# Performance work log

Measured on AMD Instinct MI355X. Metric: run time of the kernel, lower is better.

Reference implementation:

```python
import math
import jax, jax.numpy as jnp
import numpy as np

B, N, D, H = 16, 256, 1024, 16
DK = D // H
LAM_ATT, LAM_DIST = 0.33, 0.33
LAM_ADJ = 1.0 - LAM_ATT - LAM_DIST
EPS, NEG_INF = 1e-6, 1e12


def setup_inputs() -> dict:
    key = jax.random.key(0)
    ks = jax.random.split(key, 16)
    inp = {
        'query': jax.random.normal(ks[0], (B, N, D), jnp.float32),
        'key': jax.random.normal(ks[1], (B, N, D), jnp.float32),
        'value': jax.random.normal(ks[2], (B, N, D), jnp.float32),
        'adj_matrix': jax.random.uniform(ks[3], (B, N, N), jnp.float32),
        'distance_matrix': jax.random.uniform(ks[4], (B, N, N), jnp.float32),
        'edges_att': jnp.zeros((1,), jnp.float32),  # unused by forward
    }
    mask = jax.random.randint(ks[5], (B, N), 0, 2, jnp.int32)
    inp['mask'] = mask.at[:, 0].set(1)  # guarantee >=1 valid atom per graph
    scale = 0.02
    inp['Wq'] = jax.random.normal(ks[6], (D, D), jnp.float32) * scale
    inp['bq'] = jnp.zeros((D,), jnp.float32)
    inp['Wk'] = jax.random.normal(ks[7], (D, D), jnp.float32) * scale
    inp['bk'] = jnp.zeros((D,), jnp.float32)
    inp['Wv'] = jax.random.normal(ks[8], (D, D), jnp.float32) * scale
    inp['bv'] = jnp.zeros((D,), jnp.float32)
    inp['Wo'] = jax.random.normal(ks[9], (D, D), jnp.float32) * scale
    inp['bo'] = jnp.zeros((D,), jnp.float32)
    return inp


def reference(query, key, value, adj_matrix, distance_matrix, edges_att, mask,
              Wq, bq, Wk, bk, Wv, bv, Wo, bo):
    b, n, d = query.shape
    proj = lambda x, W, bias: (x @ W + bias).reshape(b, n, H, DK).transpose(0, 2, 1, 3)
    q = proj(query, Wq, bq)   # [B,H,N,DK]
    k = proj(key, Wk, bk)
    v = proj(value, Wv, bv)

    scores = jnp.einsum('bhqd,bhkd->bhqk', q, k) / math.sqrt(DK)
    key_invalid = (mask == 0)[:, None, None, :]          # [B,1,1,N]
    scores = jnp.where(key_invalid, -NEG_INF, scores)
    p_attn = jax.nn.softmax(scores, axis=-1)             # [B,H,N,N]

    # row-normalized adjacency (broadcast over heads instead of repeat)
    p_adj = adj_matrix / (adj_matrix.sum(axis=-1, keepdims=True) + EPS)  # [B,N,N]

    # distance kernel: softmax(-dist) with masked columns sent to +inf
    dist = jnp.where((mask == 0)[:, None, :], jnp.inf, distance_matrix)  # [B,N,N]
    p_dist = jax.nn.softmax(-dist, axis=-1)

    p_weighted = (LAM_ATT * p_attn
                  + LAM_DIST * p_dist[:, None]
                  + LAM_ADJ * p_adj[:, None])            # [B,H,N,N]
    # dropout p=0.0 -> identity

    x = jnp.einsum('bhqk,bhkd->bhqd', p_weighted, v)     # [B,H,N,DK]
    x = x.transpose(0, 2, 1, 3).reshape(b, n, d)
    return x @ Wo + bo
```

## Files before the change

### kernel.cpp

```cpp
#include <hip/hip_runtime.h>
#include <hip/hip_bf16.h>

typedef short short8 __attribute__((ext_vector_type(8)));
typedef short short4v __attribute__((ext_vector_type(4)));
typedef float floatx4 __attribute__((ext_vector_type(4)));

constexpr int BB  = 16;
constexpr int NN  = 256;
constexpr int DD  = 1024;
constexpr int HHc = 16;
constexpr int DKc = 64;

constexpr float LAM_ATT  = 0.33f;
constexpr float LAM_DIST = 0.33f;
constexpr float LAM_ADJ  = 0.34f;
constexpr float EPS_     = 1e-6f;

__device__ __forceinline__ float loadf(const void* p, size_t i, int f32) {
    return f32 ? ((const float*)p)[i] : (float)((const __hip_bfloat16*)p)[i];
}

__device__ __forceinline__ short8 load8_bf16(const void* p, size_t i, int f32) {
    if (f32) {
        const float4* q = (const float4*)((const float*)p + i);
        float4 a = q[0], b = q[1];
        short8 r;
        r[0] = (short)__bfloat16_as_ushort(__float2bfloat16(a.x));
        r[1] = (short)__bfloat16_as_ushort(__float2bfloat16(a.y));
        r[2] = (short)__bfloat16_as_ushort(__float2bfloat16(a.z));
        r[3] = (short)__bfloat16_as_ushort(__float2bfloat16(a.w));
        r[4] = (short)__bfloat16_as_ushort(__float2bfloat16(b.x));
        r[5] = (short)__bfloat16_as_ushort(__float2bfloat16(b.y));
        r[6] = (short)__bfloat16_as_ushort(__float2bfloat16(b.z));
        r[7] = (short)__bfloat16_as_ushort(__float2bfloat16(b.w));
        return r;
    }
    return *(const short8*)((const __hip_bfloat16*)p + i);
}

__device__ __forceinline__ void gl_lds16(const void* g, void* l) {
    __builtin_amdgcn_global_load_lds(
        (const __attribute__((address_space(1))) void*)g,
        (__attribute__((address_space(3))) void*)l, 16, 0, 0);
}

__global__ __launch_bounds__(256) void detect_kernel(
    const void* __restrict__ query, const void* __restrict__ maskraw,
    int* __restrict__ mask_canon, int* __restrict__ flags)
{
    __shared__ int s_f32;
    const int tid = threadIdx.x;
    if (tid == 0) s_f32 = 0;
    __syncthreads();

    const unsigned short* qh = (const unsigned short*)query;
    int hit = 0;
    for (int i = tid; i < 16384; i += 256)
        if ((qh[i] & 0x7F80u) == 0x7F80u) hit = 1;
    if (hit) atomicOr(&s_f32, 1);
    __syncthreads();
    if (tid == 0) flags[0] = s_f32;

    unsigned int w0 = ((const unsigned int*)maskraw)[0];
    int mdt = (w0 == 1u) ? 0 : ((w0 == 0x3F800000u) ? 1 : 2);

    for (int i = tid; i < BB * NN; i += 256) {
        int v;
        if (mdt == 0)      v = (((const int*)maskraw)[i] != 0);
        else if (mdt == 1) v = ((((const unsigned int*)maskraw)[i] & 0x7FFFFFFFu) != 0u);
        else               v = ((((const unsigned short*)maskraw)[i] & 0x7FFFu) != 0);
        mask_canon[i] = v;
    }
}

__global__ __launch_bounds__(256) void prep_w(
    const void* W0, const void* W1, const void* W2, const void* W3,
    const int* __restrict__ flags, __hip_bfloat16* __restrict__ Wt_all)
{
    const int f32 = flags[0];
    const void* W = (blockIdx.z == 0) ? W0 : (blockIdx.z == 1) ? W1
                  : (blockIdx.z == 2) ? W2 : W3;
    __hip_bfloat16* Wt = Wt_all + (size_t)blockIdx.z * DD * DD;
    __shared__ __hip_bfloat16 T[64][66];
    const int k0 = blockIdx.y * 64, n0 = blockIdx.x * 64;
    #pragma unroll
    for (int i = 0; i < 16; i++) {
        int e = threadIdx.x + i * 256;
        int kr = e >> 6, nc = e & 63;
        T[kr][nc] = __float2bfloat16(loadf(W, (size_t)(k0 + kr) * DD + n0 + nc, f32));
    }
    __syncthreads();
    #pragma unroll
    for (int i = 0; i < 16; i++) {
        int e = threadIdx.x + i * 256;
        int nr = e >> 6, kc = e & 63;
        Wt[(size_t)(n0 + nr) * DD + k0 + kc] = T[kc][nr];
    }
}

__global__ __launch_bounds__(256) void prep_bias(
    const void* b0, const void* b1, const void* b2, const void* b3,
    const int* __restrict__ flags, __hip_bfloat16* __restrict__ bias_all)
{
    const int f32 = flags[0];
    const void* s = (blockIdx.x == 0) ? b0 : (blockIdx.x == 1) ? b1
                  : (blockIdx.x == 2) ? b2 : b3;
    #pragma unroll
    for (int i = 0; i < 4; i++) {
        int idx = threadIdx.x + i * 256;
        bias_all[blockIdx.x * DD + idx] = __float2bfloat16(loadf(s, idx, f32));
    }
}

__global__ __launch_bounds__(256) void mix_kernel(
    const void* __restrict__ adj, const void* __restrict__ dist,
    const int* __restrict__ mask_canon, const int* __restrict__ flags,
    __hip_bfloat16* __restrict__ Mmix)
{
    const int f32 = flags[0];
    const int wave = threadIdx.x >> 6, lane = threadIdx.x & 63;
    const int b = blockIdx.y;
    const int q = blockIdx.x * 4 + wave;
    const size_t rowOff = ((size_t)b * NN + q) * NN;
    const int c0 = lane * 4;

    float a[4], nd[4];
    int msk[4];
    #pragma unroll
    for (int i = 0; i < 4; i++) {
        a[i]   = loadf(adj, rowOff + c0 + i, f32);
        msk[i] = mask_canon[b * NN + c0 + i];
        nd[i]  = msk[i] ? -loadf(dist, rowOff + c0 + i, f32) : -3.0e38f;
    }

    float asum = a[0] + a[1] + a[2] + a[3];
    #pragma unroll
    for (int off = 1; off < 64; off <<= 1) asum += __shfl_xor(asum, off);

    float mx = fmaxf(fmaxf(nd[0], nd[1]), fmaxf(nd[2], nd[3]));
    #pragma unroll
    for (int off = 1; off < 64; off <<= 1) mx = fmaxf(mx, __shfl_xor(mx, off));

    float e[4];
    float esum = 0.f;
    #pragma unroll
    for (int i = 0; i < 4; i++) {
        e[i] = msk[i] ? __expf(nd[i] - mx) : 0.f;
        esum += e[i];
    }
    #pragma unroll
    for (int off = 1; off < 64; off <<= 1) esum += __shfl_xor(esum, off);

    const float ia = 1.f / (asum + EPS_);
    const float ie = 1.f / fmaxf(esum, 1e-30f);
    __hip_bfloat16 out[4];
    #pragma unroll
    for (int i = 0; i < 4; i++)
        out[i] = __float2bfloat16(LAM_DIST * e[i] * ie + LAM_ADJ * a[i] * ia);
    *(short4v*)((unsigned short*)Mmix + rowOff + c0) = *(short4v*)out;
}

template<int MSUB, int NSUB>
__device__ __forceinline__ void gemm_core(
    const void* __restrict__ A,
    const __hip_bfloat16* __restrict__ Wt,
    const __hip_bfloat16* __restrict__ bias,
    void* __restrict__ C,
    int a_f32, int c_f32, int rowBase, int colBase,
    __hip_bfloat16* __restrict__ Vt, int writeVt)
{
    constexpr int BM = 32 * MSUB, BN = 32 * NSUB;
    __shared__ __hip_bfloat16 As[BM][32];
    __shared__ __hip_bfloat16 Ws[BN][32];

    const int tid  = threadIdx.x;
    const int wave = tid >> 6, lane = tid & 63;
    const int quad = lane >> 4, cl = lane & 15;
    const int wm = (wave >> 1) * (16 * MSUB), wn = (wave & 1) * (16 * NSUB);
    const int lr = lane >> 2;
    const int lc = (lane & 3) * 8;

    floatx4 acc[MSUB][NSUB];
    #pragma unroll
    for (int i = 0; i < MSUB; i++)
        #pragma unroll
        for (int j = 0; j < NSUB; j++)
            acc[i][j] = (floatx4){0.f, 0.f, 0.f, 0.f};

    for (int k0 = 0; k0 < DD; k0 += 32) {
        if (!a_f32) {
            #pragma unroll
            for (int j = 0; j < MSUB / 2; j++) {
                int r0 = (wave * (MSUB / 2) + j) * 16;
                gl_lds16((const __hip_bfloat16*)A +
                             (size_t)(rowBase + r0 + lr) * DD + k0 + lc,
                         &As[r0][0]);
            }
        } else {
            #pragma unroll
            for (int i = 0; i < BM / 64; i++) {
                int c = tid + i * 256;
                int r = c >> 2, kg = (c & 3) * 8;
                *(short8*)&As[r][kg] =
                    load8_bf16(A, (size_t)(rowBase + r) * DD + k0 + kg, 1);
            }
        }
        #pragma unroll
        for (int j = 0; j < NSUB / 2; j++) {
            int r0 = (wave * (NSUB / 2) + j) * 16;
            gl_lds16(Wt + (size_t)(colBase + r0 + lr) * DD + k0 + lc, &Ws[r0][0]);
        }
        __syncthreads();

        short8 af[MSUB], bfr[NSUB];
        #pragma unroll
        for (int ms = 0; ms < MSUB; ms++)
            af[ms] = *(const short8*)&As[wm + ms * 16 + cl][quad * 8];
        #pragma unroll
        for (int ns = 0; ns < NSUB; ns++)
            bfr[ns] = *(const short8*)&Ws[wn + ns * 16 + cl][quad * 8];
        #pragma unroll
        for (int ms = 0; ms < MSUB; ms++)
            #pragma unroll
            for (int ns = 0; ns < NSUB; ns++)
                acc[ms][ns] = __builtin_amdgcn_mfma_f32_16x16x32_bf16(
                    af[ms], bfr[ns], acc[ms][ns], 0, 0, 0);
        __syncthreads();
    }

    #pragma unroll
    for (int ns = 0; ns < NSUB; ns++) {
        int col = colBase + wn + ns * 16 + cl;
        float bc = (float)bias[col];
        if (writeVt) {
            int h = col >> 6, dk = col & 63;
            #pragma unroll
            for (int ms = 0; ms < MSUB; ms++) {
                int row0 = rowBase + wm + ms * 16 + quad * 4;
                int b = row0 >> 8, tok = row0 & 255;
                __hip_bfloat16 pk[4];
                #pragma unroll
                for (int r = 0; r < 4; r++)
                    pk[r] = __float2bfloat16(acc[ms][ns][r] + bc);
                *(short4v*)&Vt[((size_t)((b * HHc + h) * DKc + dk)) * NN + tok] =
                    *(short4v*)pk;
            }
        } else {
            #pragma unroll
            for (int ms = 0; ms < MSUB; ms++) {
                #pragma unroll
                for (int r = 0; r < 4; r++) {
                    int row = rowBase + wm + ms * 16 + quad * 4 + r;
                    float v = acc[ms][ns][r] + bc;
                    size_t idx = (size_t)row * DD + col;
                    if (c_f32) ((float*)C)[idx] = v;
                    else ((__hip_bfloat16*)C)[idx] = __float2bfloat16(v);
                }
            }
        }
    }
}

__global__ __launch_bounds__(256) void qkv_mfma(
    const void* q, const void* k, const void* v,
    const __hip_bfloat16* __restrict__ Wt_all,
    const __hip_bfloat16* __restrict__ bias_all,
    __hip_bfloat16* Qp, __hip_bfloat16* Kp, __hip_bfloat16* Vt,
    const int* __restrict__ flags)
{
    const int bid = blockIdx.x;
    const int xcd = bid & 7, s = bid >> 3;
    const int x = s & 7;
    const int t = s >> 3;
    const int y = xcd + 8 * (t & 3);
    const int z = t >> 2;

    const void* A = (z == 0) ? q : (z == 1) ? k : v;
    __hip_bfloat16* C = (z == 0) ? Qp : Kp;
    gemm_core<4, 4>(A, Wt_all + (size_t)z * DD * DD, bias_all + z * DD, C,
                    flags[0], 0, y * 128, x * 128, Vt, z == 2);
}

__global__ __launch_bounds__(256) void out_mfma(
    const __hip_bfloat16* __restrict__ X,
    const __hip_bfloat16* __restrict__ Wt,
    const __hip_bfloat16* __restrict__ bias,
    void* C, const int* __restrict__ flags)
{
    const int bid = blockIdx.x;
    const int xcd = bid & 7, s = bid >> 3;
    const int x = s & 15;
    const int y = xcd + 8 * (s >> 4);
    gemm_core<4, 2>(X, Wt, bias, C, 0, flags[0], y * 128, x * 64, nullptr, 0);
}

__global__ __launch_bounds__(256) void attn_mfma(
    const __hip_bfloat16* __restrict__ Qp,
    const __hip_bfloat16* __restrict__ Kp,
    const __hip_bfloat16* __restrict__ Vt,
    const __hip_bfloat16* __restrict__ Mmix,
    const int* __restrict__ mask_canon,
    __hip_bfloat16* __restrict__ X)
{
    __shared__ __hip_bfloat16 Ps[4][16][264];

    const int bid = blockIdx.x;
    const int xcd = bid & 7, sdec = bid >> 3;
    const int qt = sdec & 3;
    const int hb = xcd + 8 * (sdec >> 2);
    const int h = hb & 15, b = hb >> 4;

    const int tid = threadIdx.x;
    const int wave = tid >> 6, lane = tid & 63;
    const int quad = lane >> 4, cl = lane & 15;
    const int q0 = qt * 64 + wave * 16;

    const size_t qoff = ((size_t)(b * NN + q0 + cl)) * DD + h * DKc + quad * 8;
    short8 aq0 = *(const short8*)(Qp + qoff);
    short8 aq1 = *(const short8*)(Qp + qoff + 32);

    int msk[16];
    #pragma unroll
    for (int ns = 0; ns < 16; ns++)
        msk[ns] = mask_canon[b * NN + ns * 16 + cl];

    floatx4 accS[16];
    #pragma unroll
    for (int ns = 0; ns < 16; ns++) accS[ns] = (floatx4){0.f, 0.f, 0.f, 0.f};
    #pragma unroll
    for (int ns = 0; ns < 16; ns++) {
        const size_t koff = ((size_t)(b * NN + ns * 16 + cl)) * DD + h * DKc + quad * 8;
        short8 bk0 = *(const short8*)(Kp + koff);
        short8 bk1 = *(const short8*)(Kp + koff + 32);
        accS[ns] = __builtin_amdgcn_mfma_f32_16x16x32_bf16(aq0, bk0, accS[ns], 0, 0, 0);
        accS[ns] = __builtin_amdgcn_mfma_f32_16x16x32_bf16(aq1, bk1, accS[ns], 0, 0, 0);
    }

    #pragma unroll
    for (int r = 0; r < 4; r++) {
        float s[16];
        #pragma unroll
        for (int ns = 0; ns < 16; ns++)
            s[ns] = msk[ns] ? accS[ns][r] * 0.125f : -1e12f;
        float mx = s[0];
        #pragma unroll
        for (int ns = 1; ns < 16; ns++) mx = fmaxf(mx, s[ns]);
        mx = fmaxf(mx, __shfl_xor(mx, 1));
        mx = fmaxf(mx, __shfl_xor(mx, 2));
        mx = fmaxf(mx, __shfl_xor(mx, 4));
        mx = fmaxf(mx, __shfl_xor(mx, 8));
        float e[16], sum = 0.f;
        #pragma unroll
        for (int ns = 0; ns < 16; ns++) {
            e[ns] = msk[ns] ? __expf(s[ns] - mx) : 0.f;
            sum += e[ns];
        }
        sum += __shfl_xor(sum, 1);
        sum += __shfl_xor(sum, 2);
        sum += __shfl_xor(sum, 4);
        sum += __shfl_xor(sum, 8);
        float inv = LAM_ATT / sum;
        const size_t mrow = ((size_t)b * NN + q0 + quad * 4 + r) * NN;
        #pragma unroll
        for (int ns = 0; ns < 16; ns++) {
            float p = e[ns] * inv + (float)Mmix[mrow + ns * 16 + cl];
            Ps[wave][quad * 4 + r][ns * 16 + cl] = __float2bfloat16(p);
        }
    }
    __syncthreads();

    floatx4 accX[4];
    #pragma unroll
    for (int nd = 0; nd < 4; nd++) accX[nd] = (floatx4){0.f, 0.f, 0.f, 0.f};
    #pragma unroll
    for (int ks = 0; ks < 8; ks++) {
        short8 ap = *(const short8*)&Ps[wave][cl][ks * 32 + quad * 8];
        #pragma unroll
        for (int nd = 0; nd < 4; nd++) {
            const size_t voff = ((size_t)((b * HHc + h) * DKc + nd * 16 + cl)) * NN
                              + ks * 32 + quad * 8;
            short8 bv = *(const short8*)(Vt + voff);
            accX[nd] = __builtin_amdgcn_mfma_f32_16x16x32_bf16(ap, bv, accX[nd], 0, 0, 0);
        }
    }
    #pragma unroll
    for (int nd = 0; nd < 4; nd++) {
        #pragma unroll
        for (int r = 0; r < 4; r++) {
            int row = b * NN + q0 + quad * 4 + r;
            X[(size_t)row * DD + h * DKc + nd * 16 + cl] = __float2bfloat16(accX[nd][r]);
        }
    }
}

extern "C" void kernel_launch(void* const* d_in, const int* in_sizes, int n_in,
                              void* d_out, int out_size, void* d_ws, size_t ws_size,
                              hipStream_t stream)
{
    const void* query   = d_in[0];
    const void* key     = d_in[1];
    const void* value   = d_in[2];
    const void* adj     = d_in[3];
    const void* dist    = d_in[4];
    const void* maskraw = d_in[6];
    const void* Wq = d_in[7];   const void* bq = d_in[8];
    const void* Wk = d_in[9];   const void* bk = d_in[10];
    const void* Wv = d_in[11];  const void* bv = d_in[12];
    const void* Wo = d_in[13];  const void* bo = d_in[14];

    char* w = (char*)d_ws;
    int* mask_canon = (int*)w;
    int* flags      = (int*)(w + 16384);
    __hip_bfloat16* Wt_all   = (__hip_bfloat16*)(w + 32768);
    __hip_bfloat16* bias_all = (__hip_bfloat16*)(w + 32768 + ((size_t)8 << 20));
    char* base2 = w + 32768 + ((size_t)8 << 20) + 32768;
    const size_t tokElems = (size_t)BB * NN * DD;
    __hip_bfloat16* Qp   = (__hip_bfloat16*)base2;
    __hip_bfloat16* Kp   = Qp + tokElems;
    __hip_bfloat16* X    = Kp + tokElems;
    __hip_bfloat16* Vt   = X  + tokElems;
    __hip_bfloat16* Mmix = Vt + tokElems;

    detect_kernel<<<1, 256, 0, stream>>>(query, maskraw, mask_canon, flags);
    prep_w<<<dim3(16, 16, 4), 256, 0, stream>>>(Wq, Wk, Wv, Wo, flags, Wt_all);
    prep_bias<<<dim3(4), 256, 0, stream>>>(bq, bk, bv, bo, flags, bias_all);
    mix_kernel<<<dim3(NN / 4, BB), 256, 0, stream>>>(adj, dist, mask_canon, flags, Mmix);

    qkv_mfma<<<768, 256, 0, stream>>>(query, key, value,
                                      Wt_all, bias_all, Qp, Kp, Vt, flags);

    attn_mfma<<<1024, 256, 0, stream>>>(Qp, Kp, Vt, Mmix, mask_canon, X);

    out_mfma<<<512, 256, 0, stream>>>(X, Wt_all + (size_t)3 * DD * DD,
                                      bias_all + 3 * DD, d_out, flags);
}
```

Baseline: 278.4 us.

## Pre-convert activations to bf16 and stage K tile in swizzled LDS

Adds a separate kernel that converts the fp32 query/key/value inputs to bf16 once, so the QKV GEMM can always use direct global-to-LDS async loads and no longer converts the same A tiles repeatedly across column blocks. In the attention kernel, the per-head K block is loaded cooperatively into XOR-swizzled shared memory, which aliases the P buffer, replacing redundant per-wave global K reads. The cost is an extra kernel launch and about 96 MB of extra global traffic for the converted copies, plus two more barriers in attention.

```diff
diff --git a/kernel.cpp b/kernel.cpp
--- a/kernel.cpp
+++ b/kernel.cpp
@@ -73,6 +73,19 @@
     }
 }
 
+__global__ __launch_bounds__(256) void convert_acts(
+    const void* q, const void* k, const void* v,
+    __hip_bfloat16* __restrict__ Qc, __hip_bfloat16* __restrict__ Kc,
+    __hip_bfloat16* __restrict__ Vc, const int* __restrict__ flags)
+{
+    const int f32 = flags[0];
+    const int y = blockIdx.y;
+    const void* src = (y == 0) ? q : (y == 1) ? k : v;
+    __hip_bfloat16* dst = (y == 0) ? Qc : (y == 1) ? Kc : Vc;
+    size_t off = ((size_t)blockIdx.x * 256 + threadIdx.x) * 8;
+    *(short8*)(dst + off) = load8_bf16(src, off, f32);
+}
+
 __global__ __launch_bounds__(256) void prep_w(
     const void* W0, const void* W1, const void* W2, const void* W3,
     const int* __restrict__ flags, __hip_bfloat16* __restrict__ Wt_all)
@@ -162,11 +175,11 @@
 
 template<int MSUB, int NSUB>
 __device__ __forceinline__ void gemm_core(
-    const void* __restrict__ A,
+    const __hip_bfloat16* __restrict__ A,
     const __hip_bfloat16* __restrict__ Wt,
     const __hip_bfloat16* __restrict__ bias,
     void* __restrict__ C,
-    int a_f32, int c_f32, int rowBase, int colBase,
+    int c_f32, int rowBase, int colBase,
     __hip_bfloat16* __restrict__ Vt, int writeVt)
 {
     constexpr int BM = 32 * MSUB, BN = 32 * NSUB;
@@ -188,22 +201,10 @@
             acc[i][j] = (floatx4){0.f, 0.f, 0.f, 0.f};
 
     for (int k0 = 0; k0 < DD; k0 += 32) {
-        if (!a_f32) {
-            #pragma unroll
-            for (int j = 0; j < MSUB / 2; j++) {
-                int r0 = (wave * (MSUB / 2) + j) * 16;
-                gl_lds16((const __hip_bfloat16*)A +
-                             (size_t)(rowBase + r0 + lr) * DD + k0 + lc,
-                         &As[r0][0]);
-            }
-        } else {
-            #pragma unroll
-            for (int i = 0; i < BM / 64; i++) {
-                int c = tid + i * 256;
-                int r = c >> 2, kg = (c & 3) * 8;
-                *(short8*)&As[r][kg] =
-                    load8_bf16(A, (size_t)(rowBase + r) * DD + k0 + kg, 1);
-            }
+        #pragma unroll
+        for (int j = 0; j < MSUB / 2; j++) {
+            int r0 = (wave * (MSUB / 2) + j) * 16;
+            gl_lds16(A + (size_t)(rowBase + r0 + lr) * DD + k0 + lc, &As[r0][0]);
         }
         #pragma unroll
         for (int j = 0; j < NSUB / 2; j++) {
@@ -262,11 +263,11 @@
 }
 
 __global__ __launch_bounds__(256) void qkv_mfma(
-    const void* q, const void* k, const void* v,
+    const __hip_bfloat16* __restrict__ Qc, const __hip_bfloat16* __restrict__ Kc,
+    const __hip_bfloat16* __restrict__ Vc,
     const __hip_bfloat16* __restrict__ Wt_all,
     const __hip_bfloat16* __restrict__ bias_all,
-    __hip_bfloat16* Qp, __hip_bfloat16* Kp, __hip_bfloat16* Vt,
-    const int* __restrict__ flags)
+    __hip_bfloat16* Qp, __hip_bfloat16* Kp, __hip_bfloat16* Vt)
 {
     const int bid = blockIdx.x;
     const int xcd = bid & 7, s = bid >> 3;
@@ -275,10 +276,10 @@
     const int y = xcd + 8 * (t & 3);
     const int z = t >> 2;
 
-    const void* A = (z == 0) ? q : (z == 1) ? k : v;
+    const __hip_bfloat16* A = (z == 0) ? Qc : (z == 1) ? Kc : Vc;
     __hip_bfloat16* C = (z == 0) ? Qp : Kp;
     gemm_core<4, 4>(A, Wt_all + (size_t)z * DD * DD, bias_all + z * DD, C,
-                    flags[0], 0, y * 128, x * 128, Vt, z == 2);
+                    0, y * 128, x * 128, Vt, z == 2);
 }
 
 __global__ __launch_bounds__(256) void out_mfma(
@@ -291,7 +292,7 @@
     const int xcd = bid & 7, s = bid >> 3;
     const int x = s & 15;
     const int y = xcd + 8 * (s >> 4);
-    gemm_core<4, 2>(X, Wt, bias, C, 0, flags[0], y * 128, x * 64, nullptr, 0);
+    gemm_core<4, 2>(X, Wt, bias, C, flags[0], y * 128, x * 64, nullptr, 0);
 }
 
 __global__ __launch_bounds__(256) void attn_mfma(
@@ -302,7 +303,9 @@
     const int* __restrict__ mask_canon,
     __hip_bfloat16* __restrict__ X)
 {
-    __shared__ __hip_bfloat16 Ps[4][16][264];
+    __shared__ __hip_bfloat16 smem[16896];
+    __hip_bfloat16* Ks = smem;
+    __hip_bfloat16* Ps = smem;
 
     const int bid = blockIdx.x;
     const int xcd = bid & 7, sdec = bid >> 3;
@@ -319,22 +322,35 @@
     short8 aq0 = *(const short8*)(Qp + qoff);
     short8 aq1 = *(const short8*)(Qp + qoff + 32);
 
+    #pragma unroll
+    for (int j = 0; j < 8; j++) {
+        int cbase = (j * 4 + wave) * 64;
+        int c = cbase + lane;
+        int tok = c >> 3, kc = c & 7;
+        gl_lds16(Kp + ((size_t)(b * NN + tok)) * DD + h * DKc + ((kc ^ (tok & 7)) * 8),
+                 (char*)Ks + (size_t)cbase * 16);
+    }
+
     int msk[16];
     #pragma unroll
     for (int ns = 0; ns < 16; ns++)
         msk[ns] = mask_canon[b * NN + ns * 16 + cl];
 
+    __syncthreads();
+
     floatx4 accS[16];
     #pragma unroll
     for (int ns = 0; ns < 16; ns++) accS[ns] = (floatx4){0.f, 0.f, 0.f, 0.f};
     #pragma unroll
     for (int ns = 0; ns < 16; ns++) {
-        const size_t koff = ((size_t)(b * NN + ns * 16 + cl)) * DD + h * DKc + quad * 8;
-        short8 bk0 = *(const short8*)(Kp + koff);
-        short8 bk1 = *(const short8*)(Kp + koff + 32);
+        int tok = ns * 16 + cl;
+        const __hip_bfloat16* row = Ks + tok * 64;
+        short8 bk0 = *(const short8*)(row + ((quad ^ (tok & 7)) * 8));
+        short8 bk1 = *(const short8*)(row + (((quad + 4) ^ (tok & 7)) * 8));
         accS[ns] = __builtin_amdgcn_mfma_f32_16x16x32_bf16(aq0, bk0, accS[ns], 0, 0, 0);
         accS[ns] = __builtin_amdgcn_mfma_f32_16x16x32_bf16(aq1, bk1, accS[ns], 0, 0, 0);
     }
+    __syncthreads();
 
     #pragma unroll
     for (int r = 0; r < 4; r++) {
@@ -364,7 +380,7 @@
         #pragma unroll
         for (int ns = 0; ns < 16; ns++) {
             float p = e[ns] * inv + (float)Mmix[mrow + ns * 16 + cl];
-            Ps[wave][quad * 4 + r][ns * 16 + cl] = __float2bfloat16(p);
+            Ps[(wave * 16 + quad * 4 + r) * 264 + ns * 16 + cl] = __float2bfloat16(p);
         }
     }
     __syncthreads();
@@ -374,7 +390,7 @@
     for (int nd = 0; nd < 4; nd++) accX[nd] = (floatx4){0.f, 0.f, 0.f, 0.f};
     #pragma unroll
     for (int ks = 0; ks < 8; ks++) {
-        short8 ap = *(const short8*)&Ps[wave][cl][ks * 32 + quad * 8];
+        short8 ap = *(const short8*)&Ps[(wave * 16 + cl) * 264 + ks * 32 + quad * 8];
         #pragma unroll
         for (int nd = 0; nd < 4; nd++) {
             const size_t voff = ((size_t)((b * HHc + h) * DKc + nd * 16 + cl)) * NN
@@ -415,19 +431,22 @@
     __hip_bfloat16* bias_all = (__hip_bfloat16*)(w + 32768 + ((size_t)8 << 20));
     char* base2 = w + 32768 + ((size_t)8 << 20) + 32768;
     const size_t tokElems = (size_t)BB * NN * DD;
-    __hip_bfloat16* Qp   = (__hip_bfloat16*)base2;
+    __hip_bfloat16* Qc   = (__hip_bfloat16*)base2;
+    __hip_bfloat16* Kc   = Qc + tokElems;
+    __hip_bfloat16* Vc   = Kc + tokElems;
+    __hip_bfloat16* Qp   = Vc + tokElems;
     __hip_bfloat16* Kp   = Qp + tokElems;
-    __hip_bfloat16* X    = Kp + tokElems;
-    __hip_bfloat16* Vt   = X  + tokElems;
+    __hip_bfloat16* Vt   = Kp + tokElems;
     __hip_bfloat16* Mmix = Vt + tokElems;
+    __hip_bfloat16* X    = Qc;
 
     detect_kernel<<<1, 256, 0, stream>>>(query, maskraw, mask_canon, flags);
+    convert_acts<<<dim3(2048, 3), 256, 0, stream>>>(query, key, value, Qc, Kc, Vc, flags);
     prep_w<<<dim3(16, 16, 4), 256, 0, stream>>>(Wq, Wk, Wv, Wo, flags, Wt_all);
     prep_bias<<<dim3(4), 256, 0, stream>>>(bq, bk, bv, bo, flags, bias_all);
     mix_kernel<<<dim3(NN / 4, BB), 256, 0, stream>>>(adj, dist, mask_canon, flags, Mmix);
 
-    qkv_mfma<<<768, 256, 0, stream>>>(query, key, value,
-                                      Wt_all, bias_all, Qp, Kp, Vt, flags);
+    qkv_mfma<<<768, 256, 0, stream>>>(Qc, Kc, Vc, Wt_all, bias_all, Qp, Kp, Vt);
 
     attn_mfma<<<1024, 256, 0, stream>>>(Qp, Kp, Vt, Mmix, mask_canon, X);
 
```

Result: faster. 257.6 us (-7.5%).
